# Kernel tuning notes

Hardware: AMD Instinct MI355X
Metric: run time of the kernel (lower is better)

The kernel has to match this reference:

```python
import jax, jax.numpy as jnp
import numpy as np

POS_FRAC = 0.1  # typical boundary-pixel sparsity


def _bce_with_logits(x, t):
    # numerically stable binary_cross_entropy_with_logits, reduction='none'
    return jnp.maximum(x, 0.0) - x * t + jnp.log1p(jnp.exp(-jnp.abs(x)))


def setup_inputs() -> dict:
    key = jax.random.key(0)
    k1, k2 = jax.random.split(key)
    B, C, H, W = 64, 1, 512, 512
    logits = jax.random.normal(k1, (B, C, H, W), dtype=jnp.float32)
    target = (jax.random.uniform(k2, (B, C, H, W)) < POS_FRAC).astype(jnp.float32)
    return {"input": logits, "target": target}


def reference(input, target):
    # elementwise BCE map [B, C, H, W]
    bce = _bce_with_logits(input, target)

    B = target.shape[0]
    # per-sample positive fraction: t.sum() / t.numel()
    t_mean = jnp.mean(target.reshape(B, -1), axis=1)          # [B]
    beta_pos = 1.0 - t_mean                                    # weight for positive pixels
    beta_neg = t_mean                                          # weight for negative pixels
    w_pos = beta_pos.reshape(B, 1, 1, 1)
    w_neg = beta_neg.reshape(B, 1, 1, 1)

    pos_mask = target == 1.0
    neg_mask = target == 0.0

    # torch.cat(...).mean() over all positives across the batch ==
    # sum of weighted bce over positives / total positive count
    pos_sum = jnp.sum(jnp.where(pos_mask, w_pos * bce, 0.0))
    neg_sum = jnp.sum(jnp.where(neg_mask, w_neg * bce, 0.0))
    pos_cnt = jnp.sum(pos_mask.astype(jnp.float32))
    neg_cnt = jnp.sum(neg_mask.astype(jnp.float32))

    loss_pos = pos_sum / pos_cnt
    loss_neg = neg_sum / neg_cnt
    return loss_pos + loss_neg
```

## Files before the change

### kernel.cpp

```cpp
#include <hip/hip_runtime.h>
#include <hip/hip_bf16.h>


typedef float v4f __attribute__((ext_vector_type(4)));

#define S_ELEMS (512 * 512)
#define KPB 32
#define BQ (S_ELEMS / 4)
#define PBQ (BQ / KPB)
#define TPB 256
#define ITERS (PBQ / TPB)

__global__ __launch_bounds__(TPB, 4) void bce_partial(
    const v4f* __restrict__ x4, const v4f* __restrict__ t4,
    float* __restrict__ part) {
  const int blk = blockIdx.x;
  const int b = blk >> 5;
  const int k = blk & (KPB - 1);
  const long base = (long)b * BQ + (long)k * PBQ + threadIdx.x;

  v4f xv[ITERS], tv[ITERS];
#pragma unroll
  for (int i = 0; i < ITERS; ++i) {
    xv[i] = x4[base + (long)i * TPB];
    tv[i] = t4[base + (long)i * TPB];
  }

  float pos_s = 0.f, neg_s = 0.f, pos_c = 0.f;
#pragma unroll
  for (int i = 0; i < ITERS; ++i) {
#pragma unroll
    for (int c = 0; c < 4; ++c) {
      const float xc = xv[i][c];
      const float tc = tv[i][c];
      const float ax = fabsf(xc);
      const float l1p = __logf(1.f + __expf(-ax));
      const float common = fmaxf(xc, 0.f) + l1p;
      pos_s = fmaf(tc, common - xc, pos_s);
      neg_s = fmaf(1.f - tc, common, neg_s);
      pos_c += tc;
    }
  }

#pragma unroll
  for (int off = 32; off > 0; off >>= 1) {
    pos_s += __shfl_down(pos_s, off, 64);
    neg_s += __shfl_down(neg_s, off, 64);
    pos_c += __shfl_down(pos_c, off, 64);
  }

  __shared__ float sm[3][TPB / 64];
  const int lane = threadIdx.x & 63;
  const int wave = threadIdx.x >> 6;
  if (lane == 0) {
    sm[0][wave] = pos_s;
    sm[1][wave] = neg_s;
    sm[2][wave] = pos_c;
  }
  __syncthreads();
  if (threadIdx.x == 0) {
    float p = 0.f, n = 0.f, c = 0.f;
#pragma unroll
    for (int w = 0; w < TPB / 64; ++w) {
      p += sm[0][w];
      n += sm[1][w];
      c += sm[2][w];
    }
    part[blk * 3 + 0] = p;
    part[blk * 3 + 1] = n;
    part[blk * 3 + 2] = c;
  }
}

__global__ __launch_bounds__(64) void bce_final(
    const float* __restrict__ part, float* __restrict__ out, int B) {
  const int b = threadIdx.x;
  float p = 0.f, n = 0.f, c = 0.f;
  if (b < B) {
#pragma unroll 8
    for (int k = 0; k < KPB; ++k) {
      const int blk = b * KPB + k;
      p += part[blk * 3 + 0];
      n += part[blk * 3 + 1];
      c += part[blk * 3 + 2];
    }
  }
  const float tmean = c * (1.f / (float)S_ELEMS);
  float wp = (1.f - tmean) * p;
  float wn = tmean * n;
  float ct = c;
#pragma unroll
  for (int off = 32; off > 0; off >>= 1) {
    wp += __shfl_down(wp, off, 64);
    wn += __shfl_down(wn, off, 64);
    ct += __shfl_down(ct, off, 64);
  }
  if (b == 0) {
    const float pos_cnt = ct;
    const float neg_cnt = (float)B * (float)S_ELEMS - pos_cnt;
    out[0] = wp / pos_cnt + wn / neg_cnt;
  }
}

extern "C" void kernel_launch(void* const* d_in, const int* in_sizes, int n_in,
                              void* d_out, int out_size, void* d_ws, size_t ws_size,
                              hipStream_t stream) {
  const v4f* x4 = (const v4f*)d_in[0];
  const v4f* t4 = (const v4f*)d_in[1];
  float* out = (float*)d_out;
  float* part = (float*)d_ws;

  const int total = in_sizes[0];
  const int B = total / S_ELEMS;
  const int nblocks = B * KPB;

  bce_partial<<<nblocks, TPB, 0, stream>>>(x4, t4, part);
  bce_final<<<1, 64, 0, stream>>>(part, out, B);
}
```

Baseline: 145.0 us.

## Stream inputs through double-buffered LDS via async global_load_lds per wave

Replaces the register-resident bulk loads with a per-wave double-buffered pipeline that uses global_load_lds DMA to prefetch the next stage into shared memory while the current stage is computed, synchronised with manual waitcnt. It also halves the number of blocks per sample so each wave processes a longer contiguous stream. The goal is to overlap memory latency with the transcendental math and cut register pressure, at the cost of LDS traffic, fragile hand-written waitcnt encodings, and fewer blocks in flight.

Result: no change. 145.2 us (+0.1%).

```diff
diff --git a/kernel.cpp b/kernel.cpp
--- a/kernel.cpp
+++ b/kernel.cpp
@@ -5,40 +5,79 @@
 typedef float v4f __attribute__((ext_vector_type(4)));
 
 #define S_ELEMS (512 * 512)
-#define KPB 32
+#define KPB 16
 #define BQ (S_ELEMS / 4)
 #define PBQ (BQ / KPB)
 #define TPB 256
-#define ITERS (PBQ / TPB)
+#define WPB 4
+#define WF4 (PBQ / WPB)
+#define LPS 2
+#define STAGE_F4 (LPS * 64)
+#define STAGES (WF4 / STAGE_F4)
 
-__global__ __launch_bounds__(TPB, 4) void bce_partial(
+#define WAITCNT_VM4 (4 | (7 << 4) | (15 << 8))
+#define WAITCNT_VM0 (0 | (7 << 4) | (15 << 8))
+#define WAITCNT_LGKM0 (15 | (7 << 4) | (0 << 8) | (3 << 14))
+
+__device__ __forceinline__ void dma16(const v4f* g, v4f* l) {
+  __builtin_amdgcn_global_load_lds(
+      (const __attribute__((address_space(1))) void*)g,
+      (__attribute__((address_space(3))) void*)l, 16, 0, 0);
+}
+
+__global__ __launch_bounds__(TPB) void bce_partial(
     const v4f* __restrict__ x4, const v4f* __restrict__ t4,
     float* __restrict__ part) {
+  __shared__ v4f stage[WPB][2][2][STAGE_F4];
+
   const int blk = blockIdx.x;
-  const int b = blk >> 5;
-  const int k = blk & (KPB - 1);
-  const long base = (long)b * BQ + (long)k * PBQ + threadIdx.x;
+  const int b = blk / KPB;
+  const int k = blk % KPB;
+  const int wave = threadIdx.x >> 6;
+  const int lane = threadIdx.x & 63;
+  const long wbase = (long)b * BQ + (long)k * PBQ + (long)wave * WF4;
 
-  v4f xv[ITERS], tv[ITERS];
 #pragma unroll
-  for (int i = 0; i < ITERS; ++i) {
-    xv[i] = x4[base + (long)i * TPB];
-    tv[i] = t4[base + (long)i * TPB];
+  for (int j = 0; j < LPS; ++j) {
+    dma16(&x4[wbase + j * 64 + lane], &stage[wave][0][0][j * 64]);
+    dma16(&t4[wbase + j * 64 + lane], &stage[wave][0][1][j * 64]);
   }
 
   float pos_s = 0.f, neg_s = 0.f, pos_c = 0.f;
+
 #pragma unroll
-  for (int i = 0; i < ITERS; ++i) {
+  for (int s = 0; s < STAGES; ++s) {
+    const int buf = s & 1;
+    if (s + 1 < STAGES) {
+      __builtin_amdgcn_s_waitcnt(WAITCNT_LGKM0);
+      __asm__ volatile("" ::: "memory");
+      const long nb = wbase + (long)(s + 1) * STAGE_F4;
 #pragma unroll
-    for (int c = 0; c < 4; ++c) {
-      const float xc = xv[i][c];
-      const float tc = tv[i][c];
-      const float ax = fabsf(xc);
-      const float l1p = __logf(1.f + __expf(-ax));
-      const float common = fmaxf(xc, 0.f) + l1p;
-      pos_s = fmaf(tc, common - xc, pos_s);
-      neg_s = fmaf(1.f - tc, common, neg_s);
-      pos_c += tc;
+      for (int j = 0; j < LPS; ++j) {
+        dma16(&x4[nb + j * 64 + lane], &stage[wave][buf ^ 1][0][j * 64]);
+        dma16(&t4[nb + j * 64 + lane], &stage[wave][buf ^ 1][1][j * 64]);
+      }
+      __builtin_amdgcn_s_waitcnt(WAITCNT_VM4);
+    } else {
+      __builtin_amdgcn_s_waitcnt(WAITCNT_VM0);
+    }
+    __asm__ volatile("" ::: "memory");
+
+#pragma unroll
+    for (int j = 0; j < LPS; ++j) {
+      const v4f xv = stage[wave][buf][0][j * 64 + lane];
+      const v4f tv = stage[wave][buf][1][j * 64 + lane];
+#pragma unroll
+      for (int c = 0; c < 4; ++c) {
+        const float xc = xv[c];
+        const float tc = tv[c];
+        const float ax = fabsf(xc);
+        const float l1p = __logf(1.f + __expf(-ax));
+        const float common = fmaxf(xc, 0.f) + l1p;
+        pos_s = fmaf(tc, common - xc, pos_s);
+        neg_s = fmaf(1.f - tc, common, neg_s);
+        pos_c += tc;
+      }
     }
   }
 
@@ -49,9 +88,7 @@
     pos_c += __shfl_down(pos_c, off, 64);
   }
 
-  __shared__ float sm[3][TPB / 64];
-  const int lane = threadIdx.x & 63;
-  const int wave = threadIdx.x >> 6;
+  __shared__ float sm[3][WPB];
   if (lane == 0) {
     sm[0][wave] = pos_s;
     sm[1][wave] = neg_s;
@@ -61,7 +98,7 @@
   if (threadIdx.x == 0) {
     float p = 0.f, n = 0.f, c = 0.f;
 #pragma unroll
-    for (int w = 0; w < TPB / 64; ++w) {
+    for (int w = 0; w < WPB; ++w) {
       p += sm[0][w];
       n += sm[1][w];
       c += sm[2][w];
@@ -77,7 +114,7 @@
   const int b = threadIdx.x;
   float p = 0.f, n = 0.f, c = 0.f;
   if (b < B) {
-#pragma unroll 8
+#pragma unroll
     for (int k = 0; k < KPB; ++k) {
       const int blk = b * KPB + k;
       p += part[blk * 3 + 0];
```
